# Performance work log

Hardware: AMD Instinct MI355X
Metric: run time of the kernel (lower is better)

The kernel has to match this reference:

```python
import jax, jax.numpy as jnp
import numpy as np

L, N1, N2 = 2, 2, 2
E1 = sum(1 + i for i in range(N1))      # 3 first-stage DAG edges per layer
E2 = sum(N1 + i for i in range(N2))     # 5 last-stage DAG edges per layer
DIM, IN_DIM, NUM_CLASSES = 256, 128, 10
N_NODES, N_EDGES, N_GRAPHS = 8000, 128000, 64


def setup_inputs():
    key = jax.random.key(0)
    ks = jax.random.split(key, 16)
    s = 0.05  # weight scale to keep activations bounded through stacked cells
    return {
        'h': jax.random.normal(ks[0], (N_NODES, IN_DIM), jnp.float32),
        'W_emb': jax.random.normal(ks[1], (IN_DIM, DIM), jnp.float32) * s,
        'b_emb': jnp.zeros((DIM,), jnp.float32),
        'Wf_dense': jax.random.normal(ks[2], (L, E1, DIM, DIM), jnp.float32) * s,
        'bf_dense': jnp.zeros((L, E1, DIM), jnp.float32),
        'Wf_sparse': jax.random.normal(ks[3], (L, E1, DIM, DIM), jnp.float32) * s,
        'bf_sparse': jnp.zeros((L, E1, DIM), jnp.float32),
        'Wl_dense': jax.random.normal(ks[4], (L, E2, DIM, DIM), jnp.float32) * s,
        'bl_dense': jnp.zeros((L, E2, DIM), jnp.float32),
        'Wl_sparse': jax.random.normal(ks[5], (L, E2, DIM, DIM), jnp.float32) * s,
        'bl_sparse': jnp.zeros((L, E2, DIM), jnp.float32),
        'a_first': 0.001 * jax.random.normal(ks[6], (L * E1, 4), jnp.float32),
        'a_mid': 0.001 * jax.random.normal(ks[7], (L * N1, 4), jnp.float32),
        'a_last': 0.001 * jax.random.normal(ks[8], (L * E2, 4), jnp.float32),
        'C1': jax.random.normal(ks[9], (DIM, DIM // 2), jnp.float32) * s,
        'c1b': jnp.zeros((DIM // 2,), jnp.float32),
        'C2': jax.random.normal(ks[10], (DIM // 2, DIM // 4), jnp.float32) * s,
        'c2b': jnp.zeros((DIM // 4,), jnp.float32),
        'C3': jax.random.normal(ks[11], (DIM // 4, NUM_CLASSES), jnp.float32) * s,
        'c3b': jnp.zeros((NUM_CLASSES,), jnp.float32),
        'src': jax.random.randint(ks[12], (N_EDGES,), 0, N_NODES, jnp.int32),
        'dst': jax.random.randint(ks[13], (N_EDGES,), 0, N_NODES, jnp.int32),
        'graph_ids': jnp.sort(jax.random.randint(ks[14], (N_NODES,), 0, N_GRAPHS, jnp.int32)),
        'num_graphs': N_GRAPHS,
    }


def forward(h, W_emb, b_emb, Wf_dense, bf_dense, Wf_sparse, bf_sparse,
            Wl_dense, bl_dense, Wl_sparse, bl_sparse, a_first, a_mid, a_last,
            C1, c1b, C2, c2b, C3, c3b, src, dst, graph_ids, num_graphs):
    N = h.shape[0]
    deg0 = jax.ops.segment_sum(jnp.ones((src.shape[0],), h.dtype), dst, num_segments=N)
    deg = jnp.maximum(deg0, 1.0)[:, None]      # in-degree, clamped for mean
    has_nb = (deg0 > 0)[:, None]

    # DARTS softmax over candidate ops (per DAG edge)
    wf = jax.nn.softmax(a_first, axis=1)
    wm = jax.nn.softmax(a_mid, axis=1)
    wl = jax.nn.softmax(a_last, axis=1)

    def mixed(xj, w, Wd, bd, Ws, bs):
        # mixture over {f_zero, f_identity, f_dense, f_sparse}
        dense = xj @ Wd + bd
        agg = jax.ops.segment_sum(xj[src], dst, num_segments=N) / deg  # mean msg-passing
        sparse = agg @ Ws + bs
        return w[1] * xj + w[2] * dense + w[3] * sparse  # w[0]*zero omitted

    x = h @ W_emb + b_emb  # embedding (Linear, data_type='gc')
    for l in range(L):
        # first stage: DAG over N1 intermediate nodes
        states = [x]
        e = 0
        for n in range(1, N1 + 1):
            s = jnp.zeros_like(x)
            for j in range(n):
                s = s + mixed(states[j], wf[l * E1 + e], Wf_dense[l, e], bf_dense[l, e],
                              Wf_sparse[l, e], bf_sparse[l, e])
                e += 1
            states.append(jax.nn.relu(s))
        # middle stage: mixture over {identity, max, mean, sum} neighbor aggregators
        mids = []
        for n in range(N1):
            xn = states[n + 1]
            w = wm[l * N1 + n]
            msg = xn[src]
            msum = jax.ops.segment_sum(msg, dst, num_segments=N)
            mmean = msum / deg
            mmax = jnp.where(has_nb, jax.ops.segment_max(msg, dst, num_segments=N), 0.0)
            mids.append(w[0] * xn + w[1] * mmax + w[2] * mmean + w[3] * msum)
        # last stage: DAG over N2 output nodes, inputs = middle states + prior lasts
        lasts = []
        e = 0
        for n in range(N2):
            ins = mids + lasts
            s = jnp.zeros_like(x)
            for j in range(N1 + n):
                s = s + mixed(ins[j], wl[l * E2 + e], Wl_dense[l, e], bl_dense[l, e],
                              Wl_sparse[l, e], bl_sparse[l, e])
                e += 1
            lasts.append(jax.nn.relu(s))
        x = x + sum(lasts) / float(N2)  # residual cell output

    # dgl.mean_nodes readout: per-graph mean over nodes
    cnt = jnp.maximum(jax.ops.segment_sum(jnp.ones((N,), x.dtype), graph_ids,
                                          num_segments=num_graphs), 1.0)[:, None]
    hg = jax.ops.segment_sum(x, graph_ids, num_segments=num_graphs) / cnt
    # MLPReadout: 256 -> 128 -> 64 -> 10
    y = jax.nn.relu(hg @ C1 + c1b)
    y = jax.nn.relu(y @ C2 + c2b)
    return y @ C3 + c3b


def reference(h, W_emb, b_emb, Wf_dense, bf_dense, Wf_sparse, bf_sparse,
              Wl_dense, bl_dense, Wl_sparse, bl_sparse, a_first, a_mid, a_last,
              C1, c1b, C2, c2b, C3, c3b, src, dst, graph_ids, num_graphs):
    return forward(h, W_emb, b_emb, Wf_dense, bf_dense, Wf_sparse, bf_sparse,
                   Wl_dense, bl_dense, Wl_sparse, bl_sparse, a_first, a_mid, a_last,
                   C1, c1b, C2, c2b, C3, c3b, src, dst, graph_ids, num_graphs)
```

## Files before the change

kernel.cpp:

```cpp
#include <hip/hip_runtime.h>

#define N_NODES   8000
#define M_PAD     8192
#define PADR      (M_PAD - N_NODES)
#define N_EDGES   128000
#define N_GRAPHS  64
#define DIM       256
#define IN_DIM    128

typedef short bf16x8 __attribute__((ext_vector_type(8)));
typedef float f32x4 __attribute__((ext_vector_type(4)));

static __device__ __forceinline__ float bf2f(unsigned v) {
  return __uint_as_float(v << 16);
}
static __device__ __forceinline__ unsigned f2bf(float f) {
  unsigned u = __float_as_uint(f);
  return (u + 0x7fffu + ((u >> 16) & 1u)) >> 16;
}

__global__ __launch_bounds__(256) void k_init(int* __restrict__ counts,
                                              unsigned short* __restrict__ hpad,
                                              unsigned short* __restrict__ p0,
                                              unsigned short* __restrict__ p1,
                                              unsigned short* __restrict__ p2,
                                              unsigned short* __restrict__ p3) {
  int i = blockIdx.x * 256 + threadIdx.x;
  if (i < N_NODES) counts[i] = 0;
  if (i < PADR * IN_DIM) hpad[i] = 0;
  if (i < PADR * DIM) { p0[i] = 0; p1[i] = 0; p2[i] = 0; p3[i] = 0; }
}

__global__ __launch_bounds__(256) void k_count(const int* __restrict__ dst,
                                               int* __restrict__ counts) {
  int e = blockIdx.x * 256 + threadIdx.x;
  if (e < N_EDGES) atomicAdd(&counts[dst[e]], 1);
}

__global__ __launch_bounds__(256) void k_scan(const int* __restrict__ counts,
                                              int* __restrict__ row_ofs,
                                              int* __restrict__ cursor,
                                              float* __restrict__ invdeg) {
  __shared__ int chunk[256];
  const int per = (N_NODES + 255) / 256;
  int t = threadIdx.x;
  int base = t * per;
  int s = 0;
  for (int i = 0; i < per; ++i) {
    int idx = base + i;
    if (idx < N_NODES) s += counts[idx];
  }
  chunk[t] = s;
  __syncthreads();
  for (int off = 1; off < 256; off <<= 1) {
    int v = 0;
    if (t >= off) v = chunk[t - off];
    __syncthreads();
    if (t >= off) chunk[t] += v;
    __syncthreads();
  }
  int run = (t > 0) ? chunk[t - 1] : 0;
  for (int i = 0; i < per; ++i) {
    int idx = base + i;
    if (idx < N_NODES) {
      row_ofs[idx] = run;
      cursor[idx] = run;
      int c = counts[idx];
      invdeg[idx] = 1.0f / (float)(c > 1 ? c : 1);
      run += c;
    }
  }
  if (t == 0) row_ofs[N_NODES] = chunk[255];
}

__global__ __launch_bounds__(256) void k_fill(const int* __restrict__ src,
                                              const int* __restrict__ dst,
                                              int* __restrict__ cursor,
                                              int* __restrict__ csr_src) {
  int e = blockIdx.x * 256 + threadIdx.x;
  if (e < N_EDGES) {
    int p = atomicAdd(&cursor[dst[e]], 1);
    csr_src[p] = src[e];
  }
}

__global__ __launch_bounds__(64) void k_softmax(const float* __restrict__ af,
                                                const float* __restrict__ am,
                                                const float* __restrict__ al,
                                                float* __restrict__ w) {
  int t = threadIdx.x;
  const float* sp;
  float* dp;
  if (t < 6)       { sp = af + t * 4;        dp = w + t * 4; }
  else if (t < 10) { sp = am + (t - 6) * 4;  dp = w + 24 + (t - 6) * 4; }
  else if (t < 20) { sp = al + (t - 10) * 4; dp = w + 40 + (t - 10) * 4; }
  else return;
  float a0 = sp[0], a1 = sp[1], a2 = sp[2], a3 = sp[3];
  float m = fmaxf(fmaxf(a0, a1), fmaxf(a2, a3));
  float e0 = expf(a0 - m), e1 = expf(a1 - m), e2 = expf(a2 - m), e3 = expf(a3 - m);
  float si = 1.0f / (e0 + e1 + e2 + e3);
  dp[0] = e0 * si; dp[1] = e1 * si; dp[2] = e2 * si; dp[3] = e3 * si;
}

__global__ __launch_bounds__(256) void k_cvt_bf16(const float* __restrict__ in,
                                                  unsigned short* __restrict__ out,
                                                  int n) {
  int i = blockIdx.x * 256 + threadIdx.x;
  if (i < n) out[i] = (unsigned short)f2bf(in[i]);
}

__global__ __launch_bounds__(256) void k_transpose_cvt33(const float* __restrict__ Wfd,
                                                         const float* __restrict__ Wfs,
                                                         const float* __restrict__ Wld,
                                                         const float* __restrict__ Wls,
                                                         const float* __restrict__ wsoft,
                                                         unsigned short* __restrict__ out,
                                                         const float* __restrict__ W_emb,
                                                         unsigned short* __restrict__ WTe) {
  __shared__ float tile[32][33];
  int z = blockIdx.z;
  int tx = threadIdx.x & 31, ty = threadIdx.x >> 5;
  if (z == 32) {
    if (blockIdx.x >= 4) return;
    int k0 = blockIdx.x * 32, n0 = blockIdx.y * 32;
#pragma unroll
    for (int i = 0; i < 4; ++i)
      tile[ty + 8 * i][tx] = W_emb[(size_t)(k0 + ty + 8 * i) * DIM + n0 + tx];
    __syncthreads();
#pragma unroll
    for (int i = 0; i < 4; ++i)
      WTe[(size_t)(n0 + ty + 8 * i) * IN_DIM + k0 + tx] =
          (unsigned short)f2bf(tile[tx][ty + 8 * i]);
    return;
  }
  const float* in;
  float coef;
  const float* wf = wsoft;
  const float* wl = wsoft + 40;
  if (z < 6)       { in = Wfd + (size_t)z * DIM * DIM;        coef = wf[z * 4 + 2]; }
  else if (z < 12) { in = Wfs + (size_t)(z - 6) * DIM * DIM;  coef = wf[(z - 6) * 4 + 3]; }
  else if (z < 22) { in = Wld + (size_t)(z - 12) * DIM * DIM; coef = wl[(z - 12) * 4 + 2]; }
  else             { in = Wls + (size_t)(z - 22) * DIM * DIM; coef = wl[(z - 22) * 4 + 3]; }
  unsigned short* o = out + (size_t)z * DIM * DIM;
  int k0 = blockIdx.x * 32, n0 = blockIdx.y * 32;
#pragma unroll
  for (int i = 0; i < 4; ++i)
    tile[ty + 8 * i][tx] = in[(size_t)(k0 + ty + 8 * i) * DIM + n0 + tx];
  __syncthreads();
#pragma unroll
  for (int i = 0; i < 4; ++i)
    o[(size_t)(n0 + ty + 8 * i) * DIM + k0 + tx] =
        (unsigned short)f2bf(coef * tile[tx][ty + 8 * i]);
}

#define SEG_ACC(u) \
  { s0 += bf2f((u).x & 0xffffu); s1 += bf2f((u).x >> 16); \
    s2 += bf2f((u).y & 0xffffu); s3 += bf2f((u).y >> 16); }

#define MID_ACC(u) \
  { float v0 = bf2f((u).x & 0xffffu), v1 = bf2f((u).x >> 16); \
    float v2 = bf2f((u).y & 0xffffu), v3 = bf2f((u).y >> 16); \
    s0 += v0; s1 += v1; s2 += v2; s3 += v3; \
    m0 = fmaxf(m0, v0); m1 = fmaxf(m1, v1); \
    m2 = fmaxf(m2, v2); m3 = fmaxf(m3, v3); }

__global__ __launch_bounds__(256) void k_segmean_bf(const unsigned short* __restrict__ X,
                                                    const int* __restrict__ row_ofs,
                                                    const int* __restrict__ csr_src,
                                                    const float* __restrict__ invdeg,
                                                    unsigned short* __restrict__ out) {
  int node = blockIdx.x * 4 + (threadIdx.x >> 6);
  int l = threadIdx.x & 63;
  if (node >= N_NODES) return;
  int beg = row_ofs[node], end = row_ofs[node + 1];
  float s0 = 0.f, s1 = 0.f, s2 = 0.f, s3 = 0.f;
  int e = beg;
  for (; e + 8 <= end; e += 8) {
    int i0 = csr_src[e], i1 = csr_src[e + 1], i2 = csr_src[e + 2], i3 = csr_src[e + 3];
    int i4 = csr_src[e + 4], i5 = csr_src[e + 5], i6 = csr_src[e + 6], i7 = csr_src[e + 7];
    uint2 u0 = *(const uint2*)&X[(size_t)i0 * DIM + 4 * l];
    uint2 u1 = *(const uint2*)&X[(size_t)i1 * DIM + 4 * l];
    uint2 u2 = *(const uint2*)&X[(size_t)i2 * DIM + 4 * l];
    uint2 u3 = *(const uint2*)&X[(size_t)i3 * DIM + 4 * l];
    uint2 u4 = *(const uint2*)&X[(size_t)i4 * DIM + 4 * l];
    uint2 u5 = *(const uint2*)&X[(size_t)i5 * DIM + 4 * l];
    uint2 u6 = *(const uint2*)&X[(size_t)i6 * DIM + 4 * l];
    uint2 u7 = *(const uint2*)&X[(size_t)i7 * DIM + 4 * l];
    SEG_ACC(u0) SEG_ACC(u1) SEG_ACC(u2) SEG_ACC(u3)
    SEG_ACC(u4) SEG_ACC(u5) SEG_ACC(u6) SEG_ACC(u7)
  }
  for (; e + 4 <= end; e += 4) {
    int i0 = csr_src[e], i1 = csr_src[e + 1], i2 = csr_src[e + 2], i3 = csr_src[e + 3];
    uint2 u0 = *(const uint2*)&X[(size_t)i0 * DIM + 4 * l];
    uint2 u1 = *(const uint2*)&X[(size_t)i1 * DIM + 4 * l];
    uint2 u2 = *(const uint2*)&X[(size_t)i2 * DIM + 4 * l];
    uint2 u3 = *(const uint2*)&X[(size_t)i3 * DIM + 4 * l];
    SEG_ACC(u0) SEG_ACC(u1) SEG_ACC(u2) SEG_ACC(u3)
  }
  for (; e < end; ++e) {
    uint2 u = *(const uint2*)&X[(size_t)csr_src[e] * DIM + 4 * l];
    SEG_ACC(u)
  }
  float iv = invdeg[node];
  uint2 o;
  o.x = f2bf(s0 * iv) | (f2bf(s1 * iv) << 16);
  o.y = f2bf(s2 * iv) | (f2bf(s3 * iv) << 16);
  *(uint2*)&out[(size_t)node * DIM + 4 * l] = o;
}

__global__ __launch_bounds__(256) void k_segmean2_bf(const unsigned short* __restrict__ X0,
                                                     const unsigned short* __restrict__ X1,
                                                     const int* __restrict__ row_ofs,
                                                     const int* __restrict__ csr_src,
                                                     const float* __restrict__ invdeg,
                                                     unsigned short* __restrict__ out0,
                                                     unsigned short* __restrict__ out1) {
  int node = blockIdx.x * 4 + (threadIdx.x >> 6);
  int l = threadIdx.x & 63;
  if (node >= N_NODES) return;
  int beg = row_ofs[node], end = row_ofs[node + 1];
  float a0 = 0.f, a1 = 0.f, a2 = 0.f, a3 = 0.f;
  float b0 = 0.f, b1 = 0.f, b2 = 0.f, b3 = 0.f;
  int e = beg;
  for (; e + 4 <= end; e += 4) {
    size_t r0 = (size_t)csr_src[e] * DIM + 4 * l;
    size_t r1 = (size_t)csr_src[e + 1] * DIM + 4 * l;
    size_t r2 = (size_t)csr_src[e + 2] * DIM + 4 * l;
    size_t r3 = (size_t)csr_src[e + 3] * DIM + 4 * l;
    uint2 u0 = *(const uint2*)&X0[r0];
    uint2 u1 = *(const uint2*)&X0[r1];
    uint2 u2 = *(const uint2*)&X0[r2];
    uint2 u3 = *(const uint2*)&X0[r3];
    uint2 v0 = *(const uint2*)&X1[r0];
    uint2 v1 = *(const uint2*)&X1[r1];
    uint2 v2 = *(const uint2*)&X1[r2];
    uint2 v3 = *(const uint2*)&X1[r3];
    a0 += bf2f(u0.x & 0xffffu) + bf2f(u1.x & 0xffffu) + bf2f(u2.x & 0xffffu) + bf2f(u3.x & 0xffffu);
    a1 += bf2f(u0.x >> 16) + bf2f(u1.x >> 16) + bf2f(u2.x >> 16) + bf2f(u3.x >> 16);
    a2 += bf2f(u0.y & 0xffffu) + bf2f(u1.y & 0xffffu) + bf2f(u2.y & 0xffffu) + bf2f(u3.y & 0xffffu);
    a3 += bf2f(u0.y >> 16) + bf2f(u1.y >> 16) + bf2f(u2.y >> 16) + bf2f(u3.y >> 16);
    b0 += bf2f(v0.x & 0xffffu) + bf2f(v1.x & 0xffffu) + bf2f(v2.x & 0xffffu) + bf2f(v3.x & 0xffffu);
    b1 += bf2f(v0.x >> 16) + bf2f(v1.x >> 16) + bf2f(v2.x >> 16) + bf2f(v3.x >> 16);
    b2 += bf2f(v0.y & 0xffffu) + bf2f(v1.y & 0xffffu) + bf2f(v2.y & 0xffffu) + bf2f(v3.y & 0xffffu);
    b3 += bf2f(v0.y >> 16) + bf2f(v1.y >> 16) + bf2f(v2.y >> 16) + bf2f(v3.y >> 16);
  }
  for (; e < end; ++e) {
    size_t rb = (size_t)csr_src[e] * DIM + 4 * l;
    uint2 u = *(const uint2*)&X0[rb];
    uint2 v = *(const uint2*)&X1[rb];
    a0 += bf2f(u.x & 0xffffu); a1 += bf2f(u.x >> 16);
    a2 += bf2f(u.y & 0xffffu); a3 += bf2f(u.y >> 16);
    b0 += bf2f(v.x & 0xffffu); b1 += bf2f(v.x >> 16);
    b2 += bf2f(v.y & 0xffffu); b3 += bf2f(v.y >> 16);
  }
  float iv = invdeg[node];
  uint2 o;
  o.x = f2bf(a0 * iv) | (f2bf(a1 * iv) << 16);
  o.y = f2bf(a2 * iv) | (f2bf(a3 * iv) << 16);
  *(uint2*)&out0[(size_t)node * DIM + 4 * l] = o;
  o.x = f2bf(b0 * iv) | (f2bf(b1 * iv) << 16);
  o.y = f2bf(b2 * iv) | (f2bf(b3 * iv) << 16);
  *(uint2*)&out1[(size_t)node * DIM + 4 * l] = o;
}

__global__ __launch_bounds__(256) void k_segmid_bf(const unsigned short* __restrict__ Xn,
                                                   const int* __restrict__ row_ofs,
                                                   const int* __restrict__ csr_src,
                                                   const float* __restrict__ invdeg,
                                                   const float* __restrict__ wrow,
                                                   unsigned short* __restrict__ mean_out,
                                                   unsigned short* __restrict__ mids_out) {
  int node = blockIdx.x * 4 + (threadIdx.x >> 6);
  int l = threadIdx.x & 63;
  if (node >= N_NODES) return;
  int beg = row_ofs[node], end = row_ofs[node + 1];
  float s0 = 0.f, s1 = 0.f, s2 = 0.f, s3 = 0.f;
  float m0 = 0.f, m1 = 0.f, m2 = 0.f, m3 = 0.f;
  int e = beg;
  for (; e + 8 <= end; e += 8) {
    int i0 = csr_src[e], i1 = csr_src[e + 1], i2 = csr_src[e + 2], i3 = csr_src[e + 3];
    int i4 = csr_src[e + 4], i5 = csr_src[e + 5], i6 = csr_src[e + 6], i7 = csr_src[e + 7];
    uint2 u0 = *(const uint2*)&Xn[(size_t)i0 * DIM + 4 * l];
    uint2 u1 = *(const uint2*)&Xn[(size_t)i1 * DIM + 4 * l];
    uint2 u2 = *(const uint2*)&Xn[(size_t)i2 * DIM + 4 * l];
    uint2 u3 = *(const uint2*)&Xn[(size_t)i3 * DIM + 4 * l];
    uint2 u4 = *(const uint2*)&Xn[(size_t)i4 * DIM + 4 * l];
    uint2 u5 = *(const uint2*)&Xn[(size_t)i5 * DIM + 4 * l];
    uint2 u6 = *(const uint2*)&Xn[(size_t)i6 * DIM + 4 * l];
    uint2 u7 = *(const uint2*)&Xn[(size_t)i7 * DIM + 4 * l];
    MID_ACC(u0) MID_ACC(u1) MID_ACC(u2) MID_ACC(u3)
    MID_ACC(u4) MID_ACC(u5) MID_ACC(u6) MID_ACC(u7)
  }
  for (; e + 4 <= end; e += 4) {
    int i0 = csr_src[e], i1 = csr_src[e + 1], i2 = csr_src[e + 2], i3 = csr_src[e + 3];
    uint2 u0 = *(const uint2*)&Xn[(size_t)i0 * DIM + 4 * l];
    uint2 u1 = *(const uint2*)&Xn[(size_t)i1 * DIM + 4 * l];
    uint2 u2 = *(const uint2*)&Xn[(size_t)i2 * DIM + 4 * l];
    uint2 u3 = *(const uint2*)&Xn[(size_t)i3 * DIM + 4 * l];
    MID_ACC(u0) MID_ACC(u1) MID_ACC(u2) MID_ACC(u3)
  }
  for (; e < end; ++e) {
    uint2 u = *(const uint2*)&Xn[(size_t)csr_src[e] * DIM + 4 * l];
    MID_ACC(u)
  }
  float iv = invdeg[node];
  float e0 = s0 * iv, e1 = s1 * iv, e2 = s2 * iv, e3 = s3 * iv;
  if (mean_out) {
    uint2 o;
    o.x = f2bf(e0) | (f2bf(e1) << 16);
    o.y = f2bf(e2) | (f2bf(e3) << 16);
    *(uint2*)&mean_out[(size_t)node * DIM + 4 * l] = o;
  }
  float w0 = wrow[0], w1 = wrow[1], w2 = wrow[2], w3 = wrow[3];
  uint2 xu = *(const uint2*)&Xn[(size_t)node * DIM + 4 * l];
  float x0 = bf2f(xu.x & 0xffffu), x1 = bf2f(xu.x >> 16);
  float x2 = bf2f(xu.y & 0xffffu), x3 = bf2f(xu.y >> 16);
  uint2 o;
  o.x = f2bf(w0 * x0 + w1 * m0 + w2 * e0 + w3 * s0) |
        (f2bf(w0 * x1 + w1 * m1 + w2 * e1 + w3 * s1) << 16);
  o.y = f2bf(w0 * x2 + w1 * m2 + w2 * e2 + w3 * s2) |
        (f2bf(w0 * x3 + w1 * m3 + w2 * e3 + w3 * s3) << 16);
  *(uint2*)&mids_out[(size_t)node * DIM + 4 * l] = o;
}

struct GemmDescW {
  const unsigned short* A[4];
  const unsigned short* W[2][4];
  const float* b[2][4];
  const float* c[2][4];
  const unsigned short* I[2];
  const float* ic[2][2];
  const float* pre[2];
  const float* resid[2];
  const unsigned short* addl[2];
  float* out_f32[2];
  unsigned short* out_bf[2];
  int nmat, nid, K, relu[2], colshift;
};

__global__ __launch_bounds__(256) void k_gemm_mfma(GemmDescW d) {
  __shared__ __align__(16) unsigned short As[2][64][72];
  __shared__ __align__(16) unsigned short Bs[2][64][72];
  const int tid = threadIdx.x;
  const int b = blockIdx.x;
  const int cs = d.colshift;
  const int c = (b >> 3) & ((1 << cs) - 1);
  const int bm = ((b & 7) + 8 * (b >> (3 + cs))) * 64;
  const int half = c >> 2;
  const int bn = (c & 3) * 64;
  const int w = tid >> 6, l = tid & 63;
  const int wm = (w >> 1) * 32, wn = (w & 1) * 32;
  const int lr = l & 15, lk = (l >> 4) * 8;
  const int ldr = tid >> 3, ldk = (tid & 7) * 8;

  const int K = d.K;
  const int kds = (K == 256) ? 2 : 1;
  const int kmask = (1 << kds) - 1;
  const int nsteps = d.nmat << kds;

  f32x4 zero = {0.f, 0.f, 0.f, 0.f};
  f32x4 acc[2][2];
  acc[0][0] = zero; acc[0][1] = zero; acc[1][0] = zero; acc[1][1] = zero;

  auto gload = [&](int s, uint4& a0, uint4& a1, uint4& b0, uint4& b1) {
    int t = s >> kds;
    int k0 = (s & kmask) << 6;
    const unsigned short* __restrict__ A = d.A[t];
    const unsigned short* __restrict__ W = d.W[half][t];
    a0 = *(const uint4*)&A[(size_t)(bm + ldr) * K + k0 + ldk];
    a1 = *(const uint4*)&A[(size_t)(bm + ldr + 32) * K + k0 + ldk];
    b0 = *(const uint4*)&W[(size_t)(bn + ldr) * K + k0 + ldk];
    b1 = *(const uint4*)&W[(size_t)(bn + ldr + 32) * K + k0 + ldk];
  };
  auto lstore = [&](int buf, uint4 a0, uint4 a1, uint4 b0, uint4 b1) {
    *(uint4*)&As[buf][ldr][ldk] = a0;
    *(uint4*)&As[buf][ldr + 32][ldk] = a1;
    *(uint4*)&Bs[buf][ldr][ldk] = b0;
    *(uint4*)&Bs[buf][ldr + 32][ldk] = b1;
  };

  uint4 ra0, ra1, ra2, ra3;
  uint4 rb0, rb1, rb2, rb3;

  gload(0, ra0, ra1, ra2, ra3);
  gload(1, rb0, rb1, rb2, rb3);
  lstore(0, ra0, ra1, ra2, ra3);
  __syncthreads();

#define MFMA_STEP(BUF)                                                            \
  {                                                                               \
    _Pragma("unroll")                                                             \
    for (int ks = 0; ks < 2; ++ks) {                                              \
      bf16x8 a0 = *(const bf16x8*)&As[BUF][wm + lr][ks * 32 + lk];                \
      bf16x8 a1 = *(const bf16x8*)&As[BUF][wm + 16 + lr][ks * 32 + lk];           \
      bf16x8 b0 = *(const bf16x8*)&Bs[BUF][wn + lr][ks * 32 + lk];                \
      bf16x8 b1 = *(const bf16x8*)&Bs[BUF][wn + 16 + lr][ks * 32 + lk];           \
      acc[0][0] = __builtin_amdgcn_mfma_f32_16x16x32_bf16(a0, b0, acc[0][0], 0, 0, 0); \
      acc[0][1] = __builtin_amdgcn_mfma_f32_16x16x32_bf16(a0, b1, acc[0][1], 0, 0, 0); \
      acc[1][0] = __builtin_amdgcn_mfma_f32_16x16x32_bf16(a1, b0, acc[1][0], 0, 0, 0); \
      acc[1][1] = __builtin_amdgcn_mfma_f32_16x16x32_bf16(a1, b1, acc[1][1], 0, 0, 0); \
    }                                                                             \
  }

  for (int s = 0; s < nsteps; s += 2) {
    if (s + 2 < nsteps) gload(s + 2, ra0, ra1, ra2, ra3);
    MFMA_STEP(0);
    lstore(1, rb0, rb1, rb2, rb3);
    __syncthreads();
    if (s + 3 < nsteps) gload(s + 3, rb0, rb1, rb2, rb3);
    MFMA_STEP(1);
    if (s + 2 < nsteps) lstore(0, ra0, ra1, ra2, ra3);
    __syncthreads();
  }
#undef MFMA_STEP

  float bias[2] = {0.f, 0.f};
  for (int t = 0; t < d.nmat; ++t) {
    const float* bp = d.b[half][t];
    if (bp) {
      float cc = d.c[half][t] ? *d.c[half][t] : 1.0f;
      bias[0] += cc * bp[bn + wn + lr];
      bias[1] += cc * bp[bn + wn + 16 + lr];
    }
  }
  float vout[2][2][4];
#pragma unroll
  for (int m = 0; m < 2; ++m)
#pragma unroll
    for (int n = 0; n < 2; ++n)
#pragma unroll
      for (int i = 0; i < 4; ++i) vout[m][n][i] = acc[m][n][i] + bias[n];
#pragma unroll
  for (int u = 0; u < 2; ++u) {
    if (u < d.nid) {
      float icu = *d.ic[half][u];
      const unsigned short* __restrict__ I = d.I[u];
#pragma unroll
      for (int m = 0; m < 2; ++m)
#pragma unroll
        for (int n = 0; n < 2; ++n)
#pragma unroll
          for (int i = 0; i < 4; ++i) {
            int row = bm + wm + m * 16 + (l >> 4) * 4 + i;
            int col = bn + wn + n * 16 + lr;
            vout[m][n][i] += icu * bf2f(I[(size_t)row * DIM + col]);
          }
    }
  }
  const float* pre = d.pre[half];
  const float* resid = d.resid[half];
  const unsigned short* addl = d.addl[half];
  unsigned short* obf = d.out_bf[half];
  float* of32 = d.out_f32[half];
  const int do_relu = d.relu[half];
#pragma unroll
  for (int m = 0; m < 2; ++m)
#pragma unroll
    for (int n = 0; n < 2; ++n)
#pragma unroll
      for (int i = 0; i < 4; ++i) {
        int row = bm + wm + m * 16 + (l >> 4) * 4 + i;
        int col = bn + wn + n * 16 + lr;
        size_t idx = (size_t)row * DIM + col;
        float v = vout[m][n][i];
        if (pre) v += pre[idx];
        if (do_relu) v = fmaxf(v, 0.f);
        if (resid) v = resid[idx] + 0.5f * (bf2f(addl[idx]) + v);
        if (obf) obf[idx] = (unsigned short)f2bf(v);
        if (of32) of32[idx] = v;
      }
}

__global__ __launch_bounds__(256) void k_readout_mlp(const float* __restrict__ x,
                                                     const int* __restrict__ gid,
                                                     const float* __restrict__ C1,
                                                     const float* __restrict__ c1b,
                                                     const float* __restrict__ C2,
                                                     const float* __restrict__ c2b,
                                                     const float* __restrict__ C3,
                                                     const float* __restrict__ c3b,
                                                     float* __restrict__ out) {
  int g = blockIdx.x, t = threadIdx.x;
  int lo = 0, hi = N_NODES;
  while (lo < hi) { int m = (lo + hi) >> 1; if (gid[m] < g) lo = m + 1; else hi = m; }
  int beg = lo;
  lo = beg; hi = N_NODES;
  while (lo < hi) { int m = (lo + hi) >> 1; if (gid[m] <= g) lo = m + 1; else hi = m; }
  int end = lo;
  float s0 = 0.f, s1 = 0.f, s2 = 0.f, s3 = 0.f;
  float s4 = 0.f, s5 = 0.f, s6 = 0.f, s7 = 0.f;
  int i = beg;
  for (; i + 8 <= end; i += 8) {
    s0 += x[(size_t)(i + 0) * DIM + t];
    s1 += x[(size_t)(i + 1) * DIM + t];
    s2 += x[(size_t)(i + 2) * DIM + t];
    s3 += x[(size_t)(i + 3) * DIM + t];
    s4 += x[(size_t)(i + 4) * DIM + t];
    s5 += x[(size_t)(i + 5) * DIM + t];
    s6 += x[(size_t)(i + 6) * DIM + t];
    s7 += x[(size_t)(i + 7) * DIM + t];
  }
  for (; i < end; ++i) s0 += x[(size_t)i * DIM + t];
  float s = ((s0 + s1) + (s2 + s3)) + ((s4 + s5) + (s6 + s7));
  int cnt = end - beg;
  __shared__ float h0[256], h1[128], h2[64];
  h0[t] = s / (float)(cnt > 1 ? cnt : 1);
  __syncthreads();
  if (t < 128) {
    float v = c1b[t];
    for (int k = 0; k < 256; ++k) v = fmaf(h0[k], C1[k * 128 + t], v);
    h1[t] = fmaxf(v, 0.f);
  }
  __syncthreads();
  if (t < 64) {
    float v = c2b[t];
    for (int k = 0; k < 128; ++k) v = fmaf(h1[k], C2[k * 64 + t], v);
    h2[t] = fmaxf(v, 0.f);
  }
  __syncthreads();
  if (t < 10) {
    float v = c3b[t];
    for (int k = 0; k < 64; ++k) v = fmaf(h2[k], C3[k * 10 + t], v);
    out[g * 10 + t] = v;
  }
}

extern "C" void kernel_launch(void* const* d_in, const int* in_sizes, int n_in,
                              void* d_out, int out_size, void* d_ws, size_t ws_size,
                              hipStream_t stream) {
  const float* h     = (const float*)d_in[0];
  const float* W_emb = (const float*)d_in[1];
  const float* b_emb = (const float*)d_in[2];
  const float* Wf_d  = (const float*)d_in[3];
  const float* bf_d  = (const float*)d_in[4];
  const float* Wf_s  = (const float*)d_in[5];
  const float* bf_s  = (const float*)d_in[6];
  const float* Wl_d  = (const float*)d_in[7];
  const float* bl_d  = (const float*)d_in[8];
  const float* Wl_s  = (const float*)d_in[9];
  const float* bl_s  = (const float*)d_in[10];
  const float* a_first = (const float*)d_in[11];
  const float* a_mid   = (const float*)d_in[12];
  const float* a_last  = (const float*)d_in[13];
  const float* C1 = (const float*)d_in[14];
  const float* c1b = (const float*)d_in[15];
  const float* C2 = (const float*)d_in[16];
  const float* c2b = (const float*)d_in[17];
  const float* C3 = (const float*)d_in[18];
  const float* c3b = (const float*)d_in[19];
  const int* src = (const int*)d_in[20];
  const int* dst = (const int*)d_in[21];
  const int* gid = (const int*)d_in[22];
  (void)in_sizes; (void)n_in; (void)out_size; (void)ws_size;

  char* p = (char*)d_ws;
  auto alloc = [&](size_t bytes) {
    void* r = (void*)p;
    p += (bytes + 255) & ~(size_t)255;
    return r;
  };
  typedef unsigned short u16;
  const size_t NBF = (size_t)M_PAD * DIM * sizeof(u16);
  float* x_f32  = (float*)alloc((size_t)M_PAD * DIM * sizeof(float));
  float* s2part = (float*)alloc((size_t)M_PAD * DIM * sizeof(float));
  float* xpart  = (float*)alloc((size_t)M_PAD * DIM * sizeof(float));
  u16* xb    = (u16*)alloc(NBF);
  u16* s1b   = (u16*)alloc(NBF);
  u16* s2b   = (u16*)alloc(NBF);
  u16* m0b   = (u16*)alloc(NBF);
  u16* m1b   = (u16*)alloc(NBF);
  u16* l0b   = (u16*)alloc(NBF);
  u16* aggAb = (u16*)alloc(NBF);
  u16* aggBb = (u16*)alloc(NBF);
  u16* h_bf  = (u16*)alloc((size_t)M_PAD * IN_DIM * sizeof(u16));
  u16* WT    = (u16*)alloc((size_t)(DIM * IN_DIM + 32 * DIM * DIM) * sizeof(u16));
  u16* WTe   = WT;
  u16* WTfd  = WT + DIM * IN_DIM;
  u16* WTfs  = WTfd + 6 * DIM * DIM;
  u16* WTld  = WTfs + 6 * DIM * DIM;
  u16* WTls  = WTld + 10 * DIM * DIM;
  float* invdeg = (float*)alloc(N_NODES * sizeof(float));
  int* counts  = (int*)alloc(N_NODES * sizeof(int));
  int* row_ofs = (int*)alloc((N_NODES + 1) * sizeof(int));
  int* cursor  = (int*)alloc(N_NODES * sizeof(int));
  int* csr_src = (int*)alloc(N_EDGES * sizeof(int));
  float* wsoft = (float*)alloc(80 * sizeof(float));

  const int EB = (N_EDGES + 255) / 256;

  k_init<<<192, 256, 0, stream>>>(
      counts, h_bf + (size_t)N_NODES * IN_DIM,
      aggAb + (size_t)N_NODES * DIM, aggBb + (size_t)N_NODES * DIM,
      m0b + (size_t)N_NODES * DIM, m1b + (size_t)N_NODES * DIM);

  k_count<<<EB, 256, 0, stream>>>(dst, counts);
  k_scan<<<1, 256, 0, stream>>>(counts, row_ofs, cursor, invdeg);
  k_fill<<<EB, 256, 0, stream>>>(src, dst, cursor, csr_src);
  k_softmax<<<1, 64, 0, stream>>>(a_first, a_mid, a_last, wsoft);

  const float* wf = wsoft;
  const float* wm = wsoft + 24;
  const float* wl = wsoft + 40;

  k_cvt_bf16<<<(N_NODES * IN_DIM + 255) / 256, 256, 0, stream>>>(h, h_bf, N_NODES * IN_DIM);
  k_transpose_cvt33<<<dim3(8, 8, 33), 256, 0, stream>>>(Wf_d, Wf_s, Wl_d, Wl_s, wsoft,
                                                        WTfd, W_emb, WTe);

  const int GG1 = (M_PAD / 64) * 4;
  const int GG2 = (M_PAD / 64) * 8;
  const int SB = (N_NODES + 3) / 4;

  {
    GemmDescW d{};
    d.A[0] = h_bf; d.W[0][0] = WTe; d.b[0][0] = b_emb;
    d.nmat = 1; d.nid = 0; d.K = IN_DIM; d.colshift = 2;
    d.out_f32[0] = x_f32; d.out_bf[0] = xb;
    k_gemm_mfma<<<GG1, 256, 0, stream>>>(d);
  }

  for (int l = 0; l < 2; ++l) {
    auto WFD = [&](int e) { return WTfd + (size_t)(l * 3 + e) * DIM * DIM; };
    auto BFD = [&](int e) { return bf_d + (size_t)(l * 3 + e) * DIM; };
    auto WFS = [&](int e) { return WTfs + (size_t)(l * 3 + e) * DIM * DIM; };
    auto BFS = [&](int e) { return bf_s + (size_t)(l * 3 + e) * DIM; };
    auto WLD = [&](int e) { return WTld + (size_t)(l * 5 + e) * DIM * DIM; };
    auto BLD = [&](int e) { return bl_d + (size_t)(l * 5 + e) * DIM; };
    auto WLS = [&](int e) { return WTls + (size_t)(l * 5 + e) * DIM * DIM; };
    auto BLS = [&](int e) { return bl_s + (size_t)(l * 5 + e) * DIM; };
    auto WFrow = [&](int e) { return wf + (l * 3 + e) * 4; };
    auto WMrow = [&](int n) { return wm + (l * 2 + n) * 4; };
    auto WLrow = [&](int e) { return wl + (l * 5 + e) * 4; };

    k_segmean_bf<<<SB, 256, 0, stream>>>(xb, row_ofs, csr_src, invdeg, aggAb);

    {
      GemmDescW d{};
      d.A[0] = xb; d.A[1] = aggAb; d.nmat = 2; d.K = DIM; d.colshift = 3;
      d.I[0] = xb; d.nid = 1;
      d.W[0][0] = WFD(0); d.b[0][0] = BFD(0); d.c[0][0] = WFrow(0) + 2;
      d.W[0][1] = WFS(0); d.b[0][1] = BFS(0); d.c[0][1] = WFrow(0) + 3;
      d.ic[0][0] = WFrow(0) + 1; d.relu[0] = 1; d.out_bf[0] = s1b;
      d.W[1][0] = WFD(1); d.b[1][0] = BFD(1); d.c[1][0] = WFrow(1) + 2;
      d.W[1][1] = WFS(1); d.b[1][1] = BFS(1); d.c[1][1] = WFrow(1) + 3;
      d.ic[1][0] = WFrow(1) + 1; d.relu[1] = 0; d.out_f32[1] = s2part;
      k_gemm_mfma<<<GG2, 256, 0, stream>>>(d);
    }

    k_segmid_bf<<<SB, 256, 0, stream>>>(s1b, row_ofs, csr_src, invdeg, WMrow(0), aggBb, m0b);

    {
      GemmDescW d{};
      d.A[0] = s1b; d.A[1] = aggBb; d.nmat = 2; d.K = DIM; d.colshift = 2;
      d.I[0] = s1b; d.nid = 1;
      d.W[0][0] = WFD(2); d.b[0][0] = BFD(2); d.c[0][0] = WFrow(2) + 2;
      d.W[0][1] = WFS(2); d.b[0][1] = BFS(2); d.c[0][1] = WFrow(2) + 3;
      d.ic[0][0] = WFrow(2) + 1; d.pre[0] = s2part; d.relu[0] = 1; d.out_bf[0] = s2b;
      k_gemm_mfma<<<GG1, 256, 0, stream>>>(d);
    }

    k_segmid_bf<<<SB, 256, 0, stream>>>(s2b, row_ofs, csr_src, invdeg, WMrow(1), nullptr, m1b);

    k_segmean2_bf<<<SB, 256, 0, stream>>>(m0b, m1b, row_ofs, csr_src, invdeg, aggAb, aggBb);

    {
      GemmDescW d{};
      d.A[0] = m0b; d.A[1] = aggAb; d.A[2] = m1b; d.A[3] = aggBb;
      d.nmat = 4; d.K = DIM; d.colshift = 3;
      d.I[0] = m0b; d.I[1] = m1b; d.nid = 2;
      d.W[0][0] = WLD(0); d.b[0][0] = BLD(0); d.c[0][0] = WLrow(0) + 2;
      d.W[0][1] = WLS(0); d.b[0][1] = BLS(0); d.c[0][1] = WLrow(0) + 3;
      d.W[0][2] = WLD(1); d.b[0][2] = BLD(1); d.c[0][2] = WLrow(1) + 2;
      d.W[0][3] = WLS(1); d.b[0][3] = BLS(1); d.c[0][3] = WLrow(1) + 3;
      d.ic[0][0] = WLrow(0) + 1; d.ic[0][1] = WLrow(1) + 1;
      d.relu[0] = 1; d.out_bf[0] = l0b;
      d.W[1][0] = WLD(2); d.b[1][0] = BLD(2); d.c[1][0] = WLrow(2) + 2;
      d.W[1][1] = WLS(2); d.b[1][1] = BLS(2); d.c[1][1] = WLrow(2) + 3;
      d.W[1][2] = WLD(3); d.b[1][2] = BLD(3); d.c[1][2] = WLrow(3) + 2;
      d.W[1][3] = WLS(3); d.b[1][3] = BLS(3); d.c[1][3] = WLrow(3) + 3;
      d.ic[1][0] = WLrow(2) + 1; d.ic[1][1] = WLrow(3) + 1;
      d.relu[1] = 0; d.out_f32[1] = xpart;
      k_gemm_mfma<<<GG2, 256, 0, stream>>>(d);
    }

    k_segmean_bf<<<SB, 256, 0, stream>>>(l0b, row_ofs, csr_src, invdeg, s1b);

    {
      GemmDescW d{};
      d.A[0] = l0b; d.A[1] = s1b; d.nmat = 2; d.K = DIM; d.colshift = 2;
      d.I[0] = l0b; d.nid = 1;
      d.W[0][0] = WLD(4); d.b[0][0] = BLD(4); d.c[0][0] = WLrow(4) + 2;
      d.W[0][1] = WLS(4); d.b[0][1] = BLS(4); d.c[0][1] = WLrow(4) + 3;
      d.ic[0][0] = WLrow(4) + 1; d.pre[0] = xpart; d.relu[0] = 1;
      d.resid[0] = x_f32; d.addl[0] = l0b;
      d.out_f32[0] = x_f32; d.out_bf[0] = xb;
      k_gemm_mfma<<<GG1, 256, 0, stream>>>(d);
    }
  }

  k_readout_mlp<<<N_GRAPHS, 256, 0, stream>>>(x_f32, gid, C1, c1b, C2, c2b, C3, c3b,
                                              (float*)d_out);
}
```

Baseline: 324.9 us.

## Replace double-buffered LDS pipeline with single buffer and register prefetch

The GEMM main loop now uses one LDS tile for A and B instead of two. Each step stores the prefetched registers, synchronizes, issues the next global load, then runs the MFMAs. This halves shared memory per block, which may let more blocks reside per CU, but it adds a barrier per k-step and shortens the prefetch distance.

New measurement: 330.3 us. About the same (+1.7%).

```diff
diff --git a/kernel.cpp b/kernel.cpp
--- a/kernel.cpp
+++ b/kernel.cpp
@@ -339,8 +339,8 @@
 };
 
 __global__ __launch_bounds__(256) void k_gemm_mfma(GemmDescW d) {
-  __shared__ __align__(16) unsigned short As[2][64][72];
-  __shared__ __align__(16) unsigned short Bs[2][64][72];
+  __shared__ __align__(16) unsigned short As[64][72];
+  __shared__ __align__(16) unsigned short Bs[64][72];
   const int tid = threadIdx.x;
   const int b = blockIdx.x;
   const int cs = d.colshift;
@@ -372,47 +372,30 @@
     b0 = *(const uint4*)&W[(size_t)(bn + ldr) * K + k0 + ldk];
     b1 = *(const uint4*)&W[(size_t)(bn + ldr + 32) * K + k0 + ldk];
   };
-  auto lstore = [&](int buf, uint4 a0, uint4 a1, uint4 b0, uint4 b1) {
-    *(uint4*)&As[buf][ldr][ldk] = a0;
-    *(uint4*)&As[buf][ldr + 32][ldk] = a1;
-    *(uint4*)&Bs[buf][ldr][ldk] = b0;
-    *(uint4*)&Bs[buf][ldr + 32][ldk] = b1;
-  };
 
   uint4 ra0, ra1, ra2, ra3;
-  uint4 rb0, rb1, rb2, rb3;
-
   gload(0, ra0, ra1, ra2, ra3);
-  gload(1, rb0, rb1, rb2, rb3);
-  lstore(0, ra0, ra1, ra2, ra3);
-  __syncthreads();
-
-#define MFMA_STEP(BUF)                                                            \
-  {                                                                               \
-    _Pragma("unroll")                                                             \
-    for (int ks = 0; ks < 2; ++ks) {                                              \
-      bf16x8 a0 = *(const bf16x8*)&As[BUF][wm + lr][ks * 32 + lk];                \
-      bf16x8 a1 = *(const bf16x8*)&As[BUF][wm + 16 + lr][ks * 32 + lk];           \
-      bf16x8 b0 = *(const bf16x8*)&Bs[BUF][wn + lr][ks * 32 + lk];                \
-      bf16x8 b1 = *(const bf16x8*)&Bs[BUF][wn + 16 + lr][ks * 32 + lk];           \
-      acc[0][0] = __builtin_amdgcn_mfma_f32_16x16x32_bf16(a0, b0, acc[0][0], 0, 0, 0); \
-      acc[0][1] = __builtin_amdgcn_mfma_f32_16x16x32_bf16(a0, b1, acc[0][1], 0, 0, 0); \
-      acc[1][0] = __builtin_amdgcn_mfma_f32_16x16x32_bf16(a1, b0, acc[1][0], 0, 0, 0); \
-      acc[1][1] = __builtin_amdgcn_mfma_f32_16x16x32_bf16(a1, b1, acc[1][1], 0, 0, 0); \
-    }                                                                             \
-  }
-
-  for (int s = 0; s < nsteps; s += 2) {
-    if (s + 2 < nsteps) gload(s + 2, ra0, ra1, ra2, ra3);
-    MFMA_STEP(0);
-    lstore(1, rb0, rb1, rb2, rb3);
+
+  for (int s = 0; s < nsteps; ++s) {
+    *(uint4*)&As[ldr][ldk] = ra0;
+    *(uint4*)&As[ldr + 32][ldk] = ra1;
+    *(uint4*)&Bs[ldr][ldk] = ra2;
+    *(uint4*)&Bs[ldr + 32][ldk] = ra3;
     __syncthreads();
-    if (s + 3 < nsteps) gload(s + 3, rb0, rb1, rb2, rb3);
-    MFMA_STEP(1);
-    if (s + 2 < nsteps) lstore(0, ra0, ra1, ra2, ra3);
+    if (s + 1 < nsteps) gload(s + 1, ra0, ra1, ra2, ra3);
+#pragma unroll
+    for (int ks = 0; ks < 2; ++ks) {
+      bf16x8 a0 = *(const bf16x8*)&As[wm + lr][ks * 32 + lk];
+      bf16x8 a1 = *(const bf16x8*)&As[wm + 16 + lr][ks * 32 + lk];
+      bf16x8 b0 = *(const bf16x8*)&Bs[wn + lr][ks * 32 + lk];
+      bf16x8 b1 = *(const bf16x8*)&Bs[wn + 16 + lr][ks * 32 + lk];
+      acc[0][0] = __builtin_amdgcn_mfma_f32_16x16x32_bf16(a0, b0, acc[0][0], 0, 0, 0);
+      acc[0][1] = __builtin_amdgcn_mfma_f32_16x16x32_bf16(a0, b1, acc[0][1], 0, 0, 0);
+      acc[1][0] = __builtin_amdgcn_mfma_f32_16x16x32_bf16(a1, b0, acc[1][0], 0, 0, 0);
+      acc[1][1] = __builtin_amdgcn_mfma_f32_16x16x32_bf16(a1, b1, acc[1][1], 0, 0, 0);
+    }
     __syncthreads();
   }
-#undef MFMA_STEP
 
   float bias[2] = {0.f, 0.f};
   for (int t = 0; t < d.nmat; ++t) {
```
